# Optimization experiments

Measured on AMD Instinct MI355X. Metric: run time of the kernel, lower is better.

Reference implementation:

```python
import jax, jax.numpy as jnp
import numpy as np

H = 16  # attention heads


def setup_inputs() -> dict:
    key = jax.random.key(0)
    k0, k1, k2 = jax.random.split(key, 3)
    B, T, C = 2, 2048, 1024
    x = jax.random.normal(k0, (B, T, C), dtype=jnp.float32)
    W_attn = jax.random.normal(k1, (3 * C, C), dtype=jnp.float32) * 0.02
    W_proj = jax.random.normal(k2, (C, C), dtype=jnp.float32) * 0.02
    b_proj = jnp.zeros((C,), dtype=jnp.float32)
    return {"x": x, "W_attn": W_attn, "W_proj": W_proj, "b_proj": b_proj}


def reference(x, W_attn, W_proj, b_proj):
    # Eval-mode (dropout = identity), rotational_embeddings=False, flash=False path.
    B, T, C = x.shape
    d = C // H
    qkv = jnp.einsum('btc,fc->btf', x, W_attn)          # [B,T,3C] fused QKV proj
    q, k, v = jnp.split(qkv, 3, axis=-1)
    # [B,T,C] -> [B,H,T,d]
    q = q.reshape(B, T, H, d).transpose(0, 2, 1, 3)
    k = k.reshape(B, T, H, d).transpose(0, 2, 1, 3)
    v = v.reshape(B, T, H, d).transpose(0, 2, 1, 3)
    scale = 1.0 / np.sqrt(d).astype(np.float32)
    att = jnp.einsum('bhqd,bhkd->bhqk', q, k) * scale    # full TxT scores (no mask)
    att = jax.nn.softmax(att, axis=-1)
    y = jnp.einsum('bhqk,bhkd->bhqd', att, v)            # [B,H,T,d]
    y = y.transpose(0, 2, 1, 3).reshape(B, T, C)
    return jnp.einsum('btc,oc->bto', y, W_proj) + b_proj
```

## Files before the change

### kernel.cpp

```cpp
#include <hip/hip_runtime.h>
#include <hip/hip_bf16.h>
#include <stdint.h>

typedef __attribute__((ext_vector_type(8))) short bf16x8;
typedef __attribute__((ext_vector_type(4))) float f32x4;

#define MFMA16(A,B,C) __builtin_amdgcn_mfma_f32_16x16x32_bf16(A,B,C,0,0,0)


__device__ inline void gld_lds16(const __hip_bfloat16* g, __hip_bfloat16* l) {
  __builtin_amdgcn_global_load_lds(
      (const __attribute__((address_space(1))) void*)g,
      (__attribute__((address_space(3))) void*)l, 16, 0, 0);
}

__global__ __launch_bounds__(256)
void cvt_bf16(const float* __restrict__ s0, __hip_bfloat16* __restrict__ d0, int n0,
              const float* __restrict__ s1, __hip_bfloat16* __restrict__ d1, int n1,
              const float* __restrict__ s2, __hip_bfloat16* __restrict__ d2, int n2)
{
  const float* s; __hip_bfloat16* d; int n;
  if      (blockIdx.y == 0) { s = s0; d = d0; n = n0; }
  else if (blockIdx.y == 1) { s = s1; d = d1; n = n1; }
  else                      { s = s2; d = d2; n = n2; }
  int idx = (blockIdx.x * 256 + threadIdx.x) * 8;
  if (idx >= n) return;
  float4 u0 = *(const float4*)(s + idx);
  float4 u1 = *(const float4*)(s + idx + 4);
  __hip_bfloat16 t[8];
  t[0] = __float2bfloat16(u0.x); t[1] = __float2bfloat16(u0.y);
  t[2] = __float2bfloat16(u0.z); t[3] = __float2bfloat16(u0.w);
  t[4] = __float2bfloat16(u1.x); t[5] = __float2bfloat16(u1.y);
  t[6] = __float2bfloat16(u1.z); t[7] = __float2bfloat16(u1.w);
  *(int4*)(d + idx) = *(const int4*)t;
}

template<int BM, int BN, typename TC>
__global__ __launch_bounds__(256)
void gemm_bt(const __hip_bfloat16* __restrict__ A,
             const __hip_bfloat16* __restrict__ B,
             TC* __restrict__ C,
             const float* __restrict__ bias,
             __hip_bfloat16* __restrict__ vtg,
             int M, int N, int K)
{
  constexpr int MI = BM / 32;
  constexpr int NJ = BN / 32;
  constexpr int NP = (BM + BN) / 64;

  __shared__ __align__(16) __hip_bfloat16 As[BM * 32];
  __shared__ __align__(16) __hip_bfloat16 Bs[BN * 32];

  const int tid  = threadIdx.x;
  const int lane = tid & 63;
  const int w    = tid >> 6;
  const int lm   = lane & 15;
  const int g    = lane >> 4;

  const int bm = blockIdx.y * BM;
  const int bn = blockIdx.x * BN;
  const int rm = (w >> 1) * (BM / 2);
  const int cn = (w & 1) * (BN / 2);

  const f32x4 fzero = {0.0f, 0.0f, 0.0f, 0.0f};
  f32x4 acc[MI][NJ];
  for (int i = 0; i < MI; i++)
    for (int j = 0; j < NJ; j++)
      acc[i][j] = fzero;

  for (int k0 = 0; k0 < K; k0 += 32) {
    __syncthreads();
#pragma unroll
    for (int p = 0; p < NP; p++) {
      int c = tid + p * 256;
      if (c < BM * 4)
        gld_lds16(&A[(size_t)(bm + (c >> 2)) * K + k0 + (c & 3) * 8], &As[c * 8]);
      else {
        int cb = c - BM * 4;
        gld_lds16(&B[(size_t)(bn + (cb >> 2)) * K + k0 + (cb & 3) * 8], &Bs[cb * 8]);
      }
    }
    __syncthreads();

    bf16x8 af[MI], bfr[NJ];
#pragma unroll
    for (int i = 0; i < MI; i++)
      af[i] = *(const bf16x8*)&As[(rm + 16 * i + lm) * 32 + 8 * g];
#pragma unroll
    for (int j = 0; j < NJ; j++)
      bfr[j] = *(const bf16x8*)&Bs[(cn + 16 * j + lm) * 32 + 8 * g];
#pragma unroll
    for (int i = 0; i < MI; i++)
#pragma unroll
      for (int j = 0; j < NJ; j++)
        acc[i][j] = MFMA16(af[i], bfr[j], acc[i][j]);
  }

  if (vtg != nullptr && bn >= 2048) {
#pragma unroll
    for (int j = 0; j < NJ; j++) {
      int colv = bn + cn + 16 * j + lm - 2048;
      int vh = colv >> 6, dd = colv & 63;
#pragma unroll
      for (int i = 0; i < MI; i++) {
        int m0 = bm + rm + 16 * i + 4 * g;
        int bb = m0 >> 11, t0 = m0 & 2047;
        __hip_bfloat16 t4[4];
#pragma unroll
        for (int r = 0; r < 4; r++) t4[r] = __float2bfloat16(acc[i][j][r]);
        *(int2*)&vtg[((size_t)(bb * 16 + vh) * 64 + dd) * 2048 + t0] =
            *(const int2*)t4;
      }
    }
    return;
  }

  const float qs = (vtg != nullptr && bn < 1024) ? 0.125f : 1.0f;
#pragma unroll
  for (int j = 0; j < NJ; j++) {
    int coln = bn + cn + 16 * j + lm;
    float bv = bias ? bias[coln] : 0.0f;
#pragma unroll
    for (int i = 0; i < MI; i++) {
#pragma unroll
      for (int r = 0; r < 4; r++) {
        int rowm = bm + rm + 16 * i + 4 * g + r;
        float v = acc[i][j][r] * qs + bv;
        if constexpr (sizeof(TC) == 2)
          C[(size_t)rowm * N + coln] = __float2bfloat16(v);
        else
          C[(size_t)rowm * N + coln] = v;
      }
    }
  }
}

__global__ __launch_bounds__(256)
void mha(const __hip_bfloat16* __restrict__ qkv,
         const __hip_bfloat16* __restrict__ vtg,
         __hip_bfloat16* __restrict__ yout,
         __hip_bfloat16* __restrict__ po,
         float* __restrict__ pl,
         int nsteps)
{
  const int T = 2048, F = 3072, Cc = 1024;
  const int bh = blockIdx.x;
  const int b  = bh >> 4, h = bh & 15;
  const int qb0 = blockIdx.y * 128;
  const int z   = blockIdx.z;
  const int kvb = z * 32 * nsteps;

  const int tid  = threadIdx.x;
  const int lane = tid & 63;
  const int w    = tid >> 6;
  const int lm   = lane & 15;
  const int g    = lane >> 4;

  __shared__ __align__(16) __hip_bfloat16 Ks[2][32 * 64];
  __shared__ __align__(16) __hip_bfloat16 Vs[2][64 * 32];
  __shared__ __align__(16) __hip_bfloat16 Pld[4][32 * 40];

  const size_t rowbase = (size_t)b * T * F;
  const int hoff = h * 64;
  const __hip_bfloat16* Kbase = qkv + rowbase + 1024 + hoff;
  const __hip_bfloat16* Vtb   = vtg + (size_t)(b * 16 + h) * 64 * 2048;

  const int qw = qb0 + 32 * w;
  bf16x8 aq[2][2];
#pragma unroll
  for (int mt = 0; mt < 2; mt++)
#pragma unroll
    for (int kcq = 0; kcq < 2; kcq++)
      aq[mt][kcq] = *(const bf16x8*)
          &qkv[rowbase + (size_t)(qw + 16 * mt + lm) * F + hoff + 32 * kcq + 8 * g];

  const f32x4 fzero = {0.0f, 0.0f, 0.0f, 0.0f};
  f32x4 yacc[2][4];
  float lsum[2][4];
#pragma unroll
  for (int mt = 0; mt < 2; mt++) {
#pragma unroll
    for (int c = 0; c < 4; c++) yacc[mt][c] = fzero;
#pragma unroll
    for (int r = 0; r < 4; r++) lsum[mt][r] = 0.0f;
  }

  const int r0  = tid >> 3;
  const int swK = (tid & 7) ^ (r0 & 7);
  const int vdd = tid >> 2;
  const int vk  = (tid & 3) ^ ((tid >> 3) & 3);
  const int sxK = lm & 7;
  const int sxV = (lm >> 1) & 3;

  gld_lds16(Kbase + (size_t)(kvb + r0) * F + swK * 8, &Ks[0][tid * 8]);
  gld_lds16(Vtb + (size_t)vdd * 2048 + kvb + vk * 8, &Vs[0][tid * 8]);

  for (int t = 0; t < nsteps; t++) {
    const int buf = t & 1;
    __syncthreads();
    if (t + 1 < nsteps) {
      const int kvn = kvb + (t + 1) * 32;
      gld_lds16(Kbase + (size_t)(kvn + r0) * F + swK * 8, &Ks[buf ^ 1][tid * 8]);
      gld_lds16(Vtb + (size_t)vdd * 2048 + kvn + vk * 8, &Vs[buf ^ 1][tid * 8]);
    }

    f32x4 s[2][2];
#pragma unroll
    for (int c2 = 0; c2 < 2; c2++) {
      bf16x8 bk0 = *(const bf16x8*)&Ks[buf][(16 * c2 + lm) * 64 + ((0 + g) ^ sxK) * 8];
      bf16x8 bk1 = *(const bf16x8*)&Ks[buf][(16 * c2 + lm) * 64 + ((4 + g) ^ sxK) * 8];
#pragma unroll
      for (int mt = 0; mt < 2; mt++) {
        s[mt][c2] = MFMA16(aq[mt][0], bk0, fzero);
        s[mt][c2] = MFMA16(aq[mt][1], bk1, s[mt][c2]);
      }
    }

#pragma unroll
    for (int mt = 0; mt < 2; mt++)
#pragma unroll
      for (int c2 = 0; c2 < 2; c2++)
#pragma unroll
        for (int r = 0; r < 4; r++) {
          float p = __expf(s[mt][c2][r]);
          lsum[mt][r] += p;
          Pld[w][(16 * mt + 4 * g + r) * 40 + 16 * c2 + lm] = __float2bfloat16(p);
        }

    bf16x8 ap[2];
#pragma unroll
    for (int mt = 0; mt < 2; mt++)
      ap[mt] = *(const bf16x8*)&Pld[w][(16 * mt + lm) * 40 + 8 * g];
#pragma unroll
    for (int c = 0; c < 4; c++) {
      bf16x8 bv = *(const bf16x8*)&Vs[buf][(16 * c + lm) * 32 + (g ^ sxV) * 8];
#pragma unroll
      for (int mt = 0; mt < 2; mt++)
        yacc[mt][c] = MFMA16(ap[mt], bv, yacc[mt][c]);
    }
  }

#pragma unroll
  for (int mt = 0; mt < 2; mt++) {
    float lred[4];
#pragma unroll
    for (int r = 0; r < 4; r++) {
      float ls = lsum[mt][r];
      ls += __shfl_xor(ls, 1);
      ls += __shfl_xor(ls, 2);
      ls += __shfl_xor(ls, 4);
      ls += __shfl_xor(ls, 8);
      lred[r] = ls;
    }
    if (yout != nullptr) {
#pragma unroll
      for (int c = 0; c < 4; c++)
#pragma unroll
        for (int r = 0; r < 4; r++) {
          int qrow = qw + 16 * mt + 4 * g + r;
          yout[(size_t)(b * T + qrow) * Cc + hoff + 16 * c + lm] =
              __float2bfloat16(yacc[mt][c][r] / lred[r]);
        }
    } else {
      __hip_bfloat16* pz = po + (size_t)z * 4096 * 1024;
      float* plz = pl + (size_t)z * 4096 * 16;
#pragma unroll
      for (int c = 0; c < 4; c++)
#pragma unroll
        for (int r = 0; r < 4; r++) {
          int qrow = qw + 16 * mt + 4 * g + r;
          pz[(size_t)(b * T + qrow) * Cc + hoff + 16 * c + lm] =
              __float2bfloat16(yacc[mt][c][r]);
        }
      if (lm == 0)
#pragma unroll
        for (int r = 0; r < 4; r++) {
          int qrow = qw + 16 * mt + 4 * g + r;
          plz[(b * T + qrow) * 16 + h] = lred[r];
        }
    }
  }
}

__global__ __launch_bounds__(256)
void combine(const __hip_bfloat16* __restrict__ po,
             const float* __restrict__ pl,
             __hip_bfloat16* __restrict__ y)
{
  int idx = (blockIdx.x * 256 + threadIdx.x) * 8;
  int row = idx >> 10, c = idx & 1023, h = c >> 6;
  float la = pl[row * 16 + h];
  float lb = pl[4096 * 16 + row * 16 + h];
  float rinv = 1.0f / (la + lb);
  const __hip_bfloat16* pa = po + idx;
  const __hip_bfloat16* pb = po + 4096 * 1024 + idx;
  __hip_bfloat16 t[8];
#pragma unroll
  for (int j = 0; j < 8; j++)
    t[j] = __float2bfloat16(
        (__bfloat162float(pa[j]) + __bfloat162float(pb[j])) * rinv);
  *(int4*)(y + idx) = *(const int4*)t;
}

extern "C" void kernel_launch(void* const* d_in, const int* in_sizes, int n_in,
                              void* d_out, int out_size, void* d_ws, size_t ws_size,
                              hipStream_t stream)
{
  const float* x  = (const float*)d_in[0];
  const float* Wa = (const float*)d_in[1];
  const float* Wp = (const float*)d_in[2];
  const float* bp = (const float*)d_in[3];
  float* out = (float*)d_out;

  const int BT = 4096, C = 1024, F3 = 3072;
  char* ws = (char*)d_ws;
  __hip_bfloat16* qkv  = (__hip_bfloat16*)ws;
  __hip_bfloat16* vtg  = (__hip_bfloat16*)(ws + 25165824);
  __hip_bfloat16* xbf  = (__hip_bfloat16*)(ws + 33554432);
  __hip_bfloat16* yb   = xbf;
  __hip_bfloat16* Wabf = (__hip_bfloat16*)(ws + 41943040);
  __hip_bfloat16* Wpbf = (__hip_bfloat16*)(ws + 48234496);
  __hip_bfloat16* Opar = (__hip_bfloat16*)(ws + 50331648);
  float*          lpar = (float*)(ws + 67108864);
  const size_t need_split = 67633152;

  cvt_bf16<<<dim3(2048, 3), 256, 0, stream>>>(
      x, xbf, BT * C, Wa, Wabf, F3 * C, Wp, Wpbf, C * C);
  gemm_bt<128, 128, __hip_bfloat16>
      <<<dim3(F3 / 128, BT / 128), 256, 0, stream>>>(xbf, Wabf, qkv, nullptr, vtg,
                                                     BT, F3, C);
  if (ws_size >= need_split) {
    mha<<<dim3(32, 16, 2), 256, 0, stream>>>(qkv, vtg, nullptr, Opar, lpar, 32);
    combine<<<dim3(BT * C / 2048), 256, 0, stream>>>(Opar, lpar, yb);
  } else {
    mha<<<dim3(32, 16, 1), 256, 0, stream>>>(qkv, vtg, yb, nullptr, nullptr, 64);
  }
  gemm_bt<64, 128, float>
      <<<dim3(C / 128, BT / 64), 256, 0, stream>>>(yb, Wpbf, out, bp, nullptr,
                                                   BT, C, C);
}
```

Before: 209.1 us.

## Keep softmax probabilities in registers via transposed QK^T and lane permutes

The score MFMA is computed transposed (K as the A operand), so each lane holds probabilities along the key dimension. A permlane swap, or a shuffle fallback, then rearranges them straight into the A-operand layout for the PV MFMA, which removes the per-warp LDS staging buffer and its stores and loads. The log2(e) factor is folded into the Q scaling so exp2 can be used directly, and the row-sum reduction now runs across lane groups. The risk is extra permute instructions and getting the fragment layout exactly right.

```diff
diff --git a/kernel.cpp b/kernel.cpp
--- a/kernel.cpp
+++ b/kernel.cpp
@@ -4,6 +4,7 @@
 
 typedef __attribute__((ext_vector_type(8))) short bf16x8;
 typedef __attribute__((ext_vector_type(4))) float f32x4;
+typedef __attribute__((ext_vector_type(4))) unsigned u32x4;
 
 #define MFMA16(A,B,C) __builtin_amdgcn_mfma_f32_16x16x32_bf16(A,B,C,0,0,0)
 
@@ -12,6 +13,35 @@
   __builtin_amdgcn_global_load_lds(
       (const __attribute__((address_space(1))) void*)g,
       (__attribute__((address_space(3))) void*)l, 16, 0, 0);
+}
+
+__device__ inline unsigned pkbf(float a, float b) {
+  __hip_bfloat162 t = __float22bfloat162_rn(float2{a, b});
+  return *(unsigned*)&t;
+}
+
+__device__ inline void quad_mix(unsigned &a, unsigned &b) {
+#if __has_builtin(__builtin_amdgcn_permlane32_swap) && __has_builtin(__builtin_amdgcn_permlane16_swap)
+  auto r1 = __builtin_amdgcn_permlane32_swap(a, b, false, false);
+  auto r2 = __builtin_amdgcn_permlane16_swap(r1[0], r1[1], false, false);
+  a = r2[0];
+  b = r2[1];
+#else
+  int lane = (int)(threadIdx.x & 63);
+  int g = lane >> 4;
+  int lm = lane & 15;
+  int slo = (((g << 1) & 3) << 4) | lm;
+  int shi = ((((g << 1) | 1) & 3) << 4) | lm;
+  unsigned t0 = (unsigned)__shfl((int)a, slo, 64);
+  unsigned t1 = (unsigned)__shfl((int)b, slo, 64);
+  unsigned t2 = (unsigned)__shfl((int)a, shi, 64);
+  unsigned t3 = (unsigned)__shfl((int)b, shi, 64);
+  bool hi = g >= 2;
+  unsigned na = hi ? t1 : t0;
+  unsigned nb = hi ? t3 : t2;
+  a = na;
+  b = nb;
+#endif
 }
 
 __global__ __launch_bounds__(256)
@@ -115,7 +145,8 @@
     return;
   }
 
-  const float qs = (vtg != nullptr && bn < 1024) ? 0.125f : 1.0f;
+  const float qs = (vtg != nullptr && bn < 1024) ? (0.125f * 1.4426950408889634f)
+                                                 : 1.0f;
 #pragma unroll
   for (int j = 0; j < NJ; j++) {
     int coln = bn + cn + 16 * j + lm;
@@ -158,7 +189,6 @@
 
   __shared__ __align__(16) __hip_bfloat16 Ks[2][32 * 64];
   __shared__ __align__(16) __hip_bfloat16 Vs[2][64 * 32];
-  __shared__ __align__(16) __hip_bfloat16 Pld[4][32 * 40];
 
   const size_t rowbase = (size_t)b * T * F;
   const int hoff = h * 64;
@@ -170,20 +200,17 @@
 #pragma unroll
   for (int mt = 0; mt < 2; mt++)
 #pragma unroll
-    for (int kcq = 0; kcq < 2; kcq++)
-      aq[mt][kcq] = *(const bf16x8*)
-          &qkv[rowbase + (size_t)(qw + 16 * mt + lm) * F + hoff + 32 * kcq + 8 * g];
+    for (int e = 0; e < 2; e++)
+      aq[mt][e] = *(const bf16x8*)
+          &qkv[rowbase + (size_t)(qw + 16 * mt + lm) * F + hoff + 32 * e + 8 * g];
 
   const f32x4 fzero = {0.0f, 0.0f, 0.0f, 0.0f};
   f32x4 yacc[2][4];
-  float lsum[2][4];
-#pragma unroll
-  for (int mt = 0; mt < 2; mt++) {
+  float lsum[2] = {0.0f, 0.0f};
+#pragma unroll
+  for (int mt = 0; mt < 2; mt++)
 #pragma unroll
     for (int c = 0; c < 4; c++) yacc[mt][c] = fzero;
-#pragma unroll
-    for (int r = 0; r < 4; r++) lsum[mt][r] = 0.0f;
-  }
 
   const int r0  = tid >> 3;
   const int swK = (tid & 7) ^ (r0 & 7);
@@ -204,62 +231,70 @@
       gld_lds16(Vtb + (size_t)vdd * 2048 + kvn + vk * 8, &Vs[buf ^ 1][tid * 8]);
     }
 
-    f32x4 s[2][2];
+    bf16x8 kf[2][2];
 #pragma unroll
     for (int c2 = 0; c2 < 2; c2++) {
-      bf16x8 bk0 = *(const bf16x8*)&Ks[buf][(16 * c2 + lm) * 64 + ((0 + g) ^ sxK) * 8];
-      bf16x8 bk1 = *(const bf16x8*)&Ks[buf][(16 * c2 + lm) * 64 + ((4 + g) ^ sxK) * 8];
-#pragma unroll
-      for (int mt = 0; mt < 2; mt++) {
-        s[mt][c2] = MFMA16(aq[mt][0], bk0, fzero);
-        s[mt][c2] = MFMA16(aq[mt][1], bk1, s[mt][c2]);
-      }
-    }
-
-#pragma unroll
-    for (int mt = 0; mt < 2; mt++)
+      kf[c2][0] = *(const bf16x8*)&Ks[buf][(16 * c2 + lm) * 64 + ((0 + g) ^ sxK) * 8];
+      kf[c2][1] = *(const bf16x8*)&Ks[buf][(16 * c2 + lm) * 64 + ((4 + g) ^ sxK) * 8];
+    }
+#pragma unroll
+    for (int mt = 0; mt < 2; mt++) {
+      f32x4 st[2];
+#pragma unroll
+      for (int c2 = 0; c2 < 2; c2++) {
+        st[c2] = MFMA16(kf[c2][0], aq[mt][0], fzero);
+        st[c2] = MFMA16(kf[c2][1], aq[mt][1], st[c2]);
+      }
+
+      unsigned pkv[2][2];
 #pragma unroll
       for (int c2 = 0; c2 < 2; c2++)
 #pragma unroll
-        for (int r = 0; r < 4; r++) {
-          float p = __expf(s[mt][c2][r]);
-          lsum[mt][r] += p;
-          Pld[w][(16 * mt + 4 * g + r) * 40 + 16 * c2 + lm] = __float2bfloat16(p);
+        for (int u = 0; u < 2; u++) {
+          float p0 = __builtin_amdgcn_exp2f(st[c2][2 * u]);
+          float p1 = __builtin_amdgcn_exp2f(st[c2][2 * u + 1]);
+          lsum[mt] += p0 + p1;
+          pkv[c2][u] = pkbf(p0, p1);
         }
 
-    bf16x8 ap[2];
-#pragma unroll
-    for (int mt = 0; mt < 2; mt++)
-      ap[mt] = *(const bf16x8*)&Pld[w][(16 * mt + lm) * 40 + 8 * g];
-#pragma unroll
-    for (int c = 0; c < 4; c++) {
-      bf16x8 bv = *(const bf16x8*)&Vs[buf][(16 * c + lm) * 32 + (g ^ sxV) * 8];
-#pragma unroll
-      for (int mt = 0; mt < 2; mt++)
-        yacc[mt][c] = MFMA16(ap[mt], bv, yacc[mt][c]);
-    }
-  }
-
+      unsigned f0 = pkv[0][0], f2 = pkv[1][0];
+      quad_mix(f0, f2);
+      unsigned f1 = pkv[0][1], f3 = pkv[1][1];
+      quad_mix(f1, f3);
+      u32x4 fv = {f0, f1, f2, f3};
+      bf16x8 ap = __builtin_bit_cast(bf16x8, fv);
+
+#pragma unroll
+      for (int c = 0; c < 4; c++) {
+        bf16x8 bv = *(const bf16x8*)&Vs[buf][(16 * c + lm) * 32 + (g ^ sxV) * 8];
+        yacc[mt][c] = MFMA16(ap, bv, yacc[mt][c]);
+      }
+    }
+  }
+
+  float lred[2];
 #pragma unroll
   for (int mt = 0; mt < 2; mt++) {
-    float lred[4];
-#pragma unroll
-    for (int r = 0; r < 4; r++) {
-      float ls = lsum[mt][r];
-      ls += __shfl_xor(ls, 1);
-      ls += __shfl_xor(ls, 2);
-      ls += __shfl_xor(ls, 4);
-      ls += __shfl_xor(ls, 8);
-      lred[r] = ls;
-    }
+    float ls = lsum[mt];
+    ls += __shfl_xor(ls, 16);
+    ls += __shfl_xor(ls, 32);
+    lred[mt] = ls;
+  }
+
+#pragma unroll
+  for (int mt = 0; mt < 2; mt++) {
     if (yout != nullptr) {
+      float rv[4];
+#pragma unroll
+      for (int r = 0; r < 4; r++)
+        rv[r] = 1.0f / __shfl(lred[mt], 4 * g + r, 64);
 #pragma unroll
       for (int c = 0; c < 4; c++)
 #pragma unroll
         for (int r = 0; r < 4; r++) {
           int qrow = qw + 16 * mt + 4 * g + r;
           yout[(size_t)(b * T + qrow) * Cc + hoff + 16 * c + lm] =
-              __float2bfloat16(yacc[mt][c][r] / lred[r]);
+              __float2bfloat16(yacc[mt][c][r] * rv[r]);
         }
     } else {
       __hip_bfloat16* pz = po + (size_t)z * 4096 * 1024;
@@ -272,12 +307,8 @@
           pz[(size_t)(b * T + qrow) * Cc + hoff + 16 * c + lm] =
               __float2bfloat16(yacc[mt][c][r]);
         }
-      if (lm == 0)
-#pragma unroll
-        for (int r = 0; r < 4; r++) {
-          int qrow = qw + 16 * mt + 4 * g + r;
-          plz[(b * T + qrow) * 16 + h] = lred[r];
-        }
+      if (lane < 16)
+        plz[(b * T + qw + 16 * mt + lane) * 16 + h] = lred[mt];
     }
   }
 }
```

Measured after the change: 206.6 us. About the same (-1.2%).
